# Kernel optimization log

Measured on AMD Instinct MI355X. Metric: run time of the kernel, lower is better.

Reference implementation:

```python
import jax, jax.numpy as jnp
import numpy as np

B, T, N, M, L = 64, 256, 1024, 1024, 2


def setup_inputs() -> dict:
    key = jax.random.key(0)
    ks = jax.random.split(key, 5)
    scale = 1.0 / np.sqrt(M)
    x = jax.random.normal(ks[0], (B, T, N), dtype=jnp.float32)
    h = jnp.zeros((L, B, M), dtype=jnp.float32)
    c = jnp.zeros((L, B, M), dtype=jnp.float32)
    Wx = jax.random.normal(ks[1], (L, 4 * M, N), dtype=jnp.float32) * scale
    Wh = jax.random.normal(ks[2], (L, 4 * M, M), dtype=jnp.float32) * scale
    b = jnp.zeros((L, 4 * M), dtype=jnp.float32)
    return {"x": x, "h": h, "c": c, "Wx": Wx, "Wh": Wh, "b": b}


def _lstm_stack(x, h0, c0, Wx, Wh, b):
    # x: [B,T,N]; h0,c0: [L,B,M]; Wx: [L,4M,N_or_M]; Wh: [L,4M,M]; b: [L,4M]
    num_layers = Wx.shape[0]

    def step(carry, xt):
        h, c = carry  # each [L,B,M]
        inp = xt      # [B,N]
        hs, cs = [], []
        for l in range(num_layers):
            gates = inp @ Wx[l].T + h[l] @ Wh[l].T + b[l]  # [B,4M]
            i, f, g, o = jnp.split(gates, 4, axis=-1)
            i = jax.nn.sigmoid(i)
            f = jax.nn.sigmoid(f)
            g = jnp.tanh(g)
            o = jax.nn.sigmoid(o)
            cl = f * c[l] + i * g
            hl = o * jnp.tanh(cl)
            hs.append(hl)
            cs.append(cl)
            inp = hl
        h_new = jnp.stack(hs)
        c_new = jnp.stack(cs)
        return (h_new, c_new), h_new[-1]

    xt = jnp.swapaxes(x, 0, 1)  # [T,B,N]
    (h_last, c_last), outs = jax.lax.scan(step, (h0, c0), xt)
    outs = jnp.swapaxes(outs, 0, 1)  # [B,T,M]
    return outs, h_last, c_last


def reference(x, h, c, Wx, Wh, b):
    return _lstm_stack(x, h, c, Wx, Wh, b)
```

## Files before the change

### kernel.cpp

```cpp
#include <hip/hip_runtime.h>


#define T_STEPS 256
#define B_SZ 64
#define M_SZ 1024
#define N_SZ 1024
#define G4M 4096
#define BM 65536
#define RING 32
#define OUTS ((size_t)16777216)

typedef short short8 __attribute__((ext_vector_type(8)));
typedef float f32x4 __attribute__((ext_vector_type(4)));

static __device__ __forceinline__ unsigned short f2bf(float f) {
  union { float f; unsigned int u; } v; v.f = f;
  unsigned int u = v.u;
  unsigned int r = (u + 0x7FFFu + ((u >> 16) & 1u)) >> 16;
  return (unsigned short)r;
}

static __device__ __forceinline__ float sigf(float x) {
  return 1.f / (1.f + __expf(-x));
}
static __device__ __forceinline__ float tanhfast(float x) {
  return 2.f / (1.f + __expf(-2.f * x)) - 1.f;
}

static __device__ __forceinline__ short8 ld16(const unsigned short* p) {
  return *reinterpret_cast<const short8*>(p);
}

static __device__ __forceinline__ void store_wt16(void* p, f32x4 v) {
  asm volatile("global_store_dwordx4 %0, %1, off sc0 sc1" :: "v"(p), "v"(v) : "memory");
}

static __device__ __forceinline__ int xcc_id() {
  int v;
  asm volatile("s_getreg_b32 %0, hwreg(HW_REG_XCC_ID)" : "=s"(v));
  return v & 7;
}

__global__ void convert_x_kernel(const float* __restrict__ x,
                                 unsigned short* __restrict__ xb, int n4) {
  int i = blockIdx.x * blockDim.x + threadIdx.x;
  int stride = gridDim.x * blockDim.x;
  for (; i < n4; i += stride) {
    float4 v = reinterpret_cast<const float4*>(x)[i];
    ushort4 o;
    o.x = f2bf(v.x); o.y = f2bf(v.y); o.z = f2bf(v.z); o.w = f2bf(v.w);
    reinterpret_cast<ushort4*>(xb)[i] = o;
  }
}

__global__ void init_h_kernel(const float* __restrict__ h,
                              unsigned short* __restrict__ h0r,
                              unsigned short* __restrict__ h1r) {
  int i = blockIdx.x * blockDim.x + threadIdx.x;
  h0r[(size_t)(RING - 1) * BM + i] = f2bf(h[i]);
  h1r[(size_t)(RING - 1) * BM + i] = f2bf(h[BM + i]);
}

__global__ __launch_bounds__(1024, 4) void lstm_persistent(
    const unsigned short* __restrict__ xb,
    const float* __restrict__ c_in,
    const float* __restrict__ Wx,
    const float* __restrict__ Wh,
    const float* __restrict__ bias,
    float* __restrict__ out,
    unsigned short* __restrict__ h0r,
    unsigned short* __restrict__ h1r,
    int* bar) {
  __shared__ short8 sW[2][2][32][64];
  __shared__ f32x4 red1[12][64];
  __shared__ f32x4 red2[12][64];

  const int cu = blockIdx.x;
  const int tid = threadIdx.x;
  const int lane = tid & 63;
  const int w = tid >> 6;
  const int g = cu & 1;
  const int cuL = cu >> 1;
  const int src = w >> 3;
  const int kh = (w >> 2) & 1;
  const int bt = w & 3;
  const int q = lane >> 4;
  const int bl = lane & 15;
  const int bg = bt * 16 + bl;
  const int mbase = cuL * 8;
  const int xcd = xcc_id();
  const bool owner = (w < 4);

  unsigned short* hr_own = g ? h1r : h0r;

  {
    const float* baseX = Wx + (size_t)g * G4M * N_SZ;
    const float* baseH = Wh + (size_t)g * G4M * M_SZ;
#pragma unroll
    for (int mat = 0; mat < 2; ++mat) {
      const float* base = mat ? baseH : baseX;
#pragma unroll
      for (int mg = 0; mg < 2; ++mg) {
        for (int s = tid; s < 32 * 64; s += 1024) {
          int kt = s >> 6, ls = s & 63;
          int r = ls & 15;
          int k0 = kt * 32 + (ls >> 4) * 8;
          int j = (r >> 2) * 1024 + mbase + mg * 4 + (r & 3);
          const float* srcp = base + (size_t)j * 1024 + k0;
          float4 a = reinterpret_cast<const float4*>(srcp)[0];
          float4 b2 = reinterpret_cast<const float4*>(srcp)[1];
          short8 wv;
          wv[0] = (short)f2bf(a.x); wv[1] = (short)f2bf(a.y);
          wv[2] = (short)f2bf(a.z); wv[3] = (short)f2bf(a.w);
          wv[4] = (short)f2bf(b2.x); wv[5] = (short)f2bf(b2.y);
          wv[6] = (short)f2bf(b2.z); wv[7] = (short)f2bf(b2.w);
          sW[mat][mg][kt][ls] = wv;
        }
      }
    }
  }

  bool leader = false;
  if (tid == 0) {
    int expected = 0;
    leader = __hip_atomic_compare_exchange_strong(
        bar + 16 * (66 + g * 8 + xcd), &expected, cu + 1, __ATOMIC_RELAXED,
        __ATOMIC_RELAXED, __HIP_MEMORY_SCOPE_AGENT);
  }
  __syncthreads();

  float c_st[2][4] = {{0.f,0.f,0.f,0.f},{0.f,0.f,0.f,0.f}};
  float bs[2][4] = {{0.f,0.f,0.f,0.f},{0.f,0.f,0.f,0.f}};
  if (owner) {
#pragma unroll
    for (int mg = 0; mg < 2; ++mg)
#pragma unroll
      for (int e = 0; e < 4; ++e) {
        c_st[mg][e] = c_in[g * BM + bg * M_SZ + mbase + mg * 4 + e];
        bs[mg][e] = bias[g * G4M + q * 1024 + mbase + mg * 4 + e];
      }
  }

  const int ko = q * 8;
  const int ktb = kh * 16;
  int* prog0 = bar + 16 * 82;
  int* prog1 = bar + 16 * 83;

  if (g == 1 && tid == 0) {
    int guard = 0;
    while (__hip_atomic_load(prog0, __ATOMIC_RELAXED, __HIP_MEMORY_SCOPE_AGENT) < 1) {
      __builtin_amdgcn_s_sleep(1);
      if (++guard > (1 << 22)) break;
    }
  }
  __syncthreads();

  for (int k = 0; k < T_STEPS; ++k) {
    const int rs = (k + RING - 1) & (RING - 1);
    const int wslot = k & (RING - 1);

    const unsigned short* ip;
    if (src == 0) {
      ip = g ? (h0r + (size_t)wslot * BM + (size_t)bg * M_SZ)
             : (xb + ((size_t)bg * T_STEPS + k) * N_SZ);
    } else {
      ip = hr_own + (size_t)rs * BM + (size_t)bg * M_SZ;
    }

    f32x4 acc0 = { 0.f, 0.f, 0.f, 0.f };
    f32x4 acc1 = { 0.f, 0.f, 0.f, 0.f };
    if (owner) {
#pragma unroll
      for (int e = 0; e < 4; ++e) { acc0[e] = bs[0][e]; acc1[e] = bs[1][e]; }
    }

    short8 f[16];
#pragma unroll
    for (int j = 0; j < 16; ++j) f[j] = ld16(ip + (ktb + j) * 32 + ko);
    asm volatile("" ::
      "v"(f[0]), "v"(f[1]), "v"(f[2]), "v"(f[3]),
      "v"(f[4]), "v"(f[5]), "v"(f[6]), "v"(f[7]),
      "v"(f[8]), "v"(f[9]), "v"(f[10]), "v"(f[11]),
      "v"(f[12]), "v"(f[13]), "v"(f[14]), "v"(f[15]));
    __builtin_amdgcn_sched_barrier(0);
#pragma unroll
    for (int j = 0; j < 16; ++j) {
      int kt = ktb + j;
      acc0 = __builtin_amdgcn_mfma_f32_16x16x32_bf16(sW[src][0][kt][lane], f[j], acc0, 0, 0, 0);
      acc1 = __builtin_amdgcn_mfma_f32_16x16x32_bf16(sW[src][1][kt][lane], f[j], acc1, 0, 0, 0);
    }

    if (!owner) {
      int idx = (w >> 2) - 1;
      red1[idx * 4 + bt][lane] = acc0;
      red2[idx * 4 + bt][lane] = acc1;
    }
    asm volatile("s_waitcnt lgkmcnt(0)" ::: "memory");
    __builtin_amdgcn_s_barrier();
    __builtin_amdgcn_sched_barrier(0);

    if (owner) {
      f32x4 tot[2];
      tot[0] = acc0 + red1[bt][lane] + red1[4 + bt][lane] + red1[8 + bt][lane];
      tot[1] = acc1 + red2[bt][lane] + red2[4 + bt][lane] + red2[8 + bt][lane];
      float hv[2][4];
#pragma unroll
      for (int mg = 0; mg < 2; ++mg) {
#pragma unroll
        for (int e = 0; e < 4; ++e) {
          float ge_i = __shfl(tot[mg][e], bl);
          float ge_f = __shfl(tot[mg][e], bl + 16);
          float ge_g = __shfl(tot[mg][e], bl + 32);
          float ge_o = __shfl(tot[mg][e], bl + 48);
          float gi = sigf(ge_i), gf = sigf(ge_f);
          float gg = tanhfast(ge_g), go = sigf(ge_o);
          float c = gf * c_st[mg][e] + gi * gg;
          c_st[mg][e] = c;
          hv[mg][e] = go * tanhfast(c);
        }
      }
      if (q == 0) {
#pragma unroll
        for (int mg = 0; mg < 2; ++mg) {
          unsigned short* hdst = hr_own + (size_t)wslot * BM +
                                 (size_t)bg * M_SZ + mbase + mg * 4;
          unsigned long long hb =
              (unsigned long long)f2bf(hv[mg][0]) |
              ((unsigned long long)f2bf(hv[mg][1]) << 16) |
              ((unsigned long long)f2bf(hv[mg][2]) << 32) |
              ((unsigned long long)f2bf(hv[mg][3]) << 48);
          __hip_atomic_store((unsigned long long*)hdst, hb, __ATOMIC_RELAXED,
                             __HIP_MEMORY_SCOPE_AGENT);
          if (g == 1) {
            f32x4 ov = { hv[mg][0], hv[mg][1], hv[mg][2], hv[mg][3] };
            store_wt16(out + ((size_t)bg * T_STEPS + k) * M_SZ + mbase + mg * 4, ov);
          }
          if (k == T_STEPS - 1) {
            f32x4 hf = { hv[mg][0], hv[mg][1], hv[mg][2], hv[mg][3] };
            f32x4 cf = { c_st[mg][0], c_st[mg][1], c_st[mg][2], c_st[mg][3] };
            store_wt16(out + OUTS + (size_t)g * BM + (size_t)bg * M_SZ + mbase + mg * 4, hf);
            store_wt16(out + OUTS + 2 * (size_t)BM + (size_t)g * BM +
                       (size_t)bg * M_SZ + mbase + mg * 4, cf);
          }
        }
      }
    }

    {
      const int target = k + 1;
      const bool invstep = ((k & (RING - 1)) == (RING - 1));
      if (owner)
        asm volatile("s_waitcnt vmcnt(0)" ::: "memory");
      __builtin_amdgcn_s_barrier();
      if (tid == 0) {
        int* leaf = bar + 16 * (g * 16 + (cuL & 15));
        int* root = bar + 16 * (32 + g);
        int prev = __hip_atomic_fetch_add(leaf, 1, __ATOMIC_RELAXED, __HIP_MEMORY_SCOPE_AGENT);
        if ((prev & 7) == 7) {
          int pr2 = __hip_atomic_fetch_add(root, 1, __ATOMIC_RELAXED, __HIP_MEMORY_SCOPE_AGENT);
          if ((pr2 & 15) == 15) {
            __hip_atomic_store(bar + 16 * (82 + g), target, __ATOMIC_RELAXED,
                               __HIP_MEMORY_SCOPE_AGENT);
#pragma unroll
            for (int xx = 0; xx < 8; ++xx)
              __hip_atomic_store(bar + 16 * (34 + g * 8 + xx), target,
                                 __ATOMIC_RELAXED, __HIP_MEMORY_SCOPE_AGENT);
          }
        }
        int guard = 0;
        int* rel  = bar + 16 * (34 + g * 8 + xcd);
        int* relB = bar + 16 * (50 + g * 8 + xcd);
        while (__hip_atomic_load(rel, __ATOMIC_RELAXED, __HIP_MEMORY_SCOPE_AGENT) < target) {
          __builtin_amdgcn_s_sleep(1);
          if (++guard > (1 << 22)) break;
        }
        if (g == 1 && k + 1 < T_STEPS) {
          int need = (k + 2 < T_STEPS + 1) ? (k + 2) : T_STEPS;
          guard = 0;
          while (__hip_atomic_load(prog0, __ATOMIC_RELAXED, __HIP_MEMORY_SCOPE_AGENT) < need) {
            __builtin_amdgcn_s_sleep(1);
            if (++guard > (1 << 22)) break;
          }
        } else if (g == 0 && k + 1 >= RING && k + 1 < T_STEPS) {
          int need = k - 30;
          guard = 0;
          while (__hip_atomic_load(prog1, __ATOMIC_RELAXED, __HIP_MEMORY_SCOPE_AGENT) < need) {
            __builtin_amdgcn_s_sleep(1);
            if (++guard > (1 << 22)) break;
          }
        }
        if (invstep) {
          if (leader) {
            asm volatile("buffer_inv sc0 sc1\n\ts_waitcnt vmcnt(0)" ::: "memory");
            __hip_atomic_store(relB, target, __ATOMIC_RELAXED, __HIP_MEMORY_SCOPE_AGENT);
          } else {
            guard = 0;
            while (__hip_atomic_load(relB, __ATOMIC_RELAXED, __HIP_MEMORY_SCOPE_AGENT) < target) {
              __builtin_amdgcn_s_sleep(1);
              if (++guard > (1 << 22)) break;
            }
            asm volatile("buffer_inv sc0\n\ts_waitcnt vmcnt(0)" ::: "memory");
          }
        }
      }
      __builtin_amdgcn_s_barrier();
      __builtin_amdgcn_sched_barrier(0);
    }
  }
}

extern "C" void kernel_launch(void* const* d_in, const int* in_sizes, int n_in,
                              void* d_out, int out_size, void* d_ws, size_t ws_size,
                              hipStream_t stream) {
  (void)in_sizes; (void)n_in; (void)out_size; (void)ws_size;
  const float* x  = (const float*)d_in[0];
  const float* h  = (const float*)d_in[1];
  const float* c  = (const float*)d_in[2];
  const float* Wx = (const float*)d_in[3];
  const float* Wh = (const float*)d_in[4];
  const float* b  = (const float*)d_in[5];
  float* out = (float*)d_out;

  char* ws = (char*)d_ws;
  int* bar = (int*)ws;
  unsigned short* h0r = (unsigned short*)(ws + 8192);
  unsigned short* h1r = (unsigned short*)(ws + 8192 + (size_t)RING * BM * 2);
  unsigned short* xb  = (unsigned short*)(ws + 8192 + (size_t)RING * BM * 4);

  (void)hipMemsetAsync(ws, 0, 8192, stream);
  convert_x_kernel<<<2048, 256, 0, stream>>>(x, xb, (B_SZ * T_STEPS * N_SZ) / 4);
  init_h_kernel<<<256, 256, 0, stream>>>(h, h0r, h1r);
  lstm_persistent<<<256, 1024, 0, stream>>>(xb, c, Wx, Wh, b, out, h0r, h1r, bar);
}
```

Measured before the change: 3.151 ms.

## Split LSTM into four pipelined domains with separate input-projection producers

```diff
diff --git a/kernel.cpp b/kernel.cpp
--- a/kernel.cpp
+++ b/kernel.cpp
@@ -8,6 +8,7 @@
 #define G4M 4096
 #define BM 65536
 #define RING 32
+#define GSTRIDE ((size_t)262144)
 #define OUTS ((size_t)16777216)
 
 typedef short short8 __attribute__((ext_vector_type(8)));
@@ -19,22 +20,22 @@
   unsigned int r = (u + 0x7FFFu + ((u >> 16) & 1u)) >> 16;
   return (unsigned short)r;
 }
-
+static __device__ __forceinline__ float bf2f(unsigned int us) {
+  union { unsigned int u; float f; } v; v.u = (us & 0xFFFFu) << 16;
+  return v.f;
+}
 static __device__ __forceinline__ float sigf(float x) {
   return 1.f / (1.f + __expf(-x));
 }
 static __device__ __forceinline__ float tanhfast(float x) {
   return 2.f / (1.f + __expf(-2.f * x)) - 1.f;
 }
-
 static __device__ __forceinline__ short8 ld16(const unsigned short* p) {
   return *reinterpret_cast<const short8*>(p);
 }
-
 static __device__ __forceinline__ void store_wt16(void* p, f32x4 v) {
   asm volatile("global_store_dwordx4 %0, %1, off sc0 sc1" :: "v"(p), "v"(v) : "memory");
 }
-
 static __device__ __forceinline__ int xcc_id() {
   int v;
   asm volatile("s_getreg_b32 %0, hwreg(HW_REG_XCC_ID)" : "=s"(v));
@@ -61,7 +62,7 @@
   h1r[(size_t)(RING - 1) * BM + i] = f2bf(h[BM + i]);
 }
 
-__global__ __launch_bounds__(1024, 4) void lstm_persistent(
+__global__ __launch_bounds__(1024, 4) void lstm_pipeline(
     const unsigned short* __restrict__ xb,
     const float* __restrict__ c_in,
     const float* __restrict__ Wx,
@@ -70,52 +71,43 @@
     float* __restrict__ out,
     unsigned short* __restrict__ h0r,
     unsigned short* __restrict__ h1r,
+    unsigned short* __restrict__ g0x,
+    unsigned short* __restrict__ g1x,
     int* bar) {
-  __shared__ short8 sW[2][2][32][64];
-  __shared__ f32x4 red1[12][64];
-  __shared__ f32x4 red2[12][64];
+  __shared__ short8 sW[4][32][64];
 
   const int cu = blockIdx.x;
   const int tid = threadIdx.x;
   const int lane = tid & 63;
   const int w = tid >> 6;
-  const int g = cu & 1;
-  const int cuL = cu >> 1;
-  const int src = w >> 3;
-  const int kh = (w >> 2) & 1;
-  const int bt = w & 3;
+  const int dom = cu & 3;
+  const int cuD = cu >> 2;
+  const int lay = dom & 1;
+  const bool serial = (dom < 2);
   const int q = lane >> 4;
   const int bl = lane & 15;
-  const int bg = bt * 16 + bl;
-  const int mbase = cuL * 8;
+  const int ko = q * 8;
   const int xcd = xcc_id();
-  const bool owner = (w < 4);
-
-  unsigned short* hr_own = g ? h1r : h0r;
 
   {
-    const float* baseX = Wx + (size_t)g * G4M * N_SZ;
-    const float* baseH = Wh + (size_t)g * G4M * M_SZ;
-#pragma unroll
-    for (int mat = 0; mat < 2; ++mat) {
-      const float* base = mat ? baseH : baseX;
-#pragma unroll
-      for (int mg = 0; mg < 2; ++mg) {
-        for (int s = tid; s < 32 * 64; s += 1024) {
-          int kt = s >> 6, ls = s & 63;
-          int r = ls & 15;
-          int k0 = kt * 32 + (ls >> 4) * 8;
-          int j = (r >> 2) * 1024 + mbase + mg * 4 + (r & 3);
-          const float* srcp = base + (size_t)j * 1024 + k0;
-          float4 a = reinterpret_cast<const float4*>(srcp)[0];
-          float4 b2 = reinterpret_cast<const float4*>(srcp)[1];
-          short8 wv;
-          wv[0] = (short)f2bf(a.x); wv[1] = (short)f2bf(a.y);
-          wv[2] = (short)f2bf(a.z); wv[3] = (short)f2bf(a.w);
-          wv[4] = (short)f2bf(b2.x); wv[5] = (short)f2bf(b2.y);
-          wv[6] = (short)f2bf(b2.z); wv[7] = (short)f2bf(b2.w);
-          sW[mat][mg][kt][ls] = wv;
-        }
+    const float* base = serial ? (Wh + (size_t)lay * G4M * M_SZ)
+                               : (Wx + (size_t)lay * G4M * N_SZ);
+#pragma unroll
+    for (int idx4 = 0; idx4 < 4; ++idx4) {
+      for (int s = tid; s < 32 * 64; s += 1024) {
+        int kt = s >> 6, ls = s & 63, r = ls & 15;
+        int k0 = kt * 32 + (ls >> 4) * 8;
+        int j = serial ? (idx4 * 1024 + cuD * 16 + r)
+                       : (cuD * 64 + idx4 * 16 + r);
+        const float* sp = base + (size_t)j * 1024 + k0;
+        float4 a = reinterpret_cast<const float4*>(sp)[0];
+        float4 b2 = reinterpret_cast<const float4*>(sp)[1];
+        short8 wv;
+        wv[0] = (short)f2bf(a.x); wv[1] = (short)f2bf(a.y);
+        wv[2] = (short)f2bf(a.z); wv[3] = (short)f2bf(a.w);
+        wv[4] = (short)f2bf(b2.x); wv[5] = (short)f2bf(b2.y);
+        wv[6] = (short)f2bf(b2.z); wv[7] = (short)f2bf(b2.w);
+        sW[idx4][kt][ls] = wv;
       }
     }
   }
@@ -124,172 +116,241 @@
   if (tid == 0) {
     int expected = 0;
     leader = __hip_atomic_compare_exchange_strong(
-        bar + 16 * (66 + g * 8 + xcd), &expected, cu + 1, __ATOMIC_RELAXED,
+        bar + 16 * (100 + dom * 8 + xcd), &expected, cu + 1, __ATOMIC_RELAXED,
         __ATOMIC_RELAXED, __HIP_MEMORY_SCOPE_AGENT);
   }
   __syncthreads();
 
-  float c_st[2][4] = {{0.f,0.f,0.f,0.f},{0.f,0.f,0.f,0.f}};
-  float bs[2][4] = {{0.f,0.f,0.f,0.f},{0.f,0.f,0.f,0.f}};
-  if (owner) {
-#pragma unroll
-    for (int mg = 0; mg < 2; ++mg)
-#pragma unroll
-      for (int e = 0; e < 4; ++e) {
-        c_st[mg][e] = c_in[g * BM + bg * M_SZ + mbase + mg * 4 + e];
-        bs[mg][e] = bias[g * G4M + q * 1024 + mbase + mg * 4 + e];
-      }
-  }
-
-  const int ko = q * 8;
-  const int ktb = kh * 16;
-  int* prog0 = bar + 16 * 82;
-  int* prog1 = bar + 16 * 83;
-
-  if (g == 1 && tid == 0) {
+  int* prog0  = bar + 16 * 132;
+  int* prog1  = bar + 16 * 133;
+  int* progB0 = bar + 16 * 134;
+  int* progB1 = bar + 16 * 135;
+
+  if (tid == 0) {
     int guard = 0;
-    while (__hip_atomic_load(prog0, __ATOMIC_RELAXED, __HIP_MEMORY_SCOPE_AGENT) < 1) {
-      __builtin_amdgcn_s_sleep(1);
-      if (++guard > (1 << 22)) break;
+    if (dom == 0) {
+      while (__hip_atomic_load(progB0, __ATOMIC_RELAXED, __HIP_MEMORY_SCOPE_AGENT) < 1) {
+        __builtin_amdgcn_s_sleep(1); if (++guard > (1 << 22)) break;
+      }
+    } else if (dom == 1) {
+      while (__hip_atomic_load(progB1, __ATOMIC_RELAXED, __HIP_MEMORY_SCOPE_AGENT) < 1) {
+        __builtin_amdgcn_s_sleep(1); if (++guard > (1 << 22)) break;
+      }
+    } else if (dom == 3) {
+      while (__hip_atomic_load(prog0, __ATOMIC_RELAXED, __HIP_MEMORY_SCOPE_AGENT) < 1) {
+        __builtin_amdgcn_s_sleep(1); if (++guard > (1 << 22)) break;
+      }
     }
   }
   __syncthreads();
 
-  for (int k = 0; k < T_STEPS; ++k) {
-    const int rs = (k + RING - 1) & (RING - 1);
-    const int wslot = k & (RING - 1);
-
-    const unsigned short* ip;
-    if (src == 0) {
-      ip = g ? (h0r + (size_t)wslot * BM + (size_t)bg * M_SZ)
-             : (xb + ((size_t)bg * T_STEPS + k) * N_SZ);
-    } else {
-      ip = hr_own + (size_t)rs * BM + (size_t)bg * M_SZ;
+  int* myleaf = bar + 16 * (dom * 8 + (cuD & 7));
+  int* myroot = bar + 16 * (32 + dom);
+  int* myprog = bar + 16 * (132 + dom);
+  int* rel  = bar + 16 * (36 + dom * 8 + xcd);
+  int* relB = bar + 16 * (68 + dom * 8 + xcd);
+
+  if (serial) {
+    unsigned short* hr = lay ? h1r : h0r;
+    unsigned short* gr = lay ? g1x : g0x;
+    const int bt = w & 3;
+    const int bg = bt * 16 + bl;
+    const int mloc = cuD * 16 + q * 4;
+    float c_st[4] = {0.f, 0.f, 0.f, 0.f};
+    if (w < 4) {
+#pragma unroll
+      for (int e = 0; e < 4; ++e)
+        c_st[e] = c_in[lay * BM + bg * M_SZ + mloc + e];
     }
 
-    f32x4 acc0 = { 0.f, 0.f, 0.f, 0.f };
-    f32x4 acc1 = { 0.f, 0.f, 0.f, 0.f };
-    if (owner) {
-#pragma unroll
-      for (int e = 0; e < 4; ++e) { acc0[e] = bs[0][e]; acc1[e] = bs[1][e]; }
-    }
-
-    short8 f[16];
-#pragma unroll
-    for (int j = 0; j < 16; ++j) f[j] = ld16(ip + (ktb + j) * 32 + ko);
-    asm volatile("" ::
-      "v"(f[0]), "v"(f[1]), "v"(f[2]), "v"(f[3]),
-      "v"(f[4]), "v"(f[5]), "v"(f[6]), "v"(f[7]),
-      "v"(f[8]), "v"(f[9]), "v"(f[10]), "v"(f[11]),
-      "v"(f[12]), "v"(f[13]), "v"(f[14]), "v"(f[15]));
-    __builtin_amdgcn_sched_barrier(0);
-#pragma unroll
-    for (int j = 0; j < 16; ++j) {
-      int kt = ktb + j;
-      acc0 = __builtin_amdgcn_mfma_f32_16x16x32_bf16(sW[src][0][kt][lane], f[j], acc0, 0, 0, 0);
-      acc1 = __builtin_amdgcn_mfma_f32_16x16x32_bf16(sW[src][1][kt][lane], f[j], acc1, 0, 0, 0);
-    }
-
-    if (!owner) {
-      int idx = (w >> 2) - 1;
-      red1[idx * 4 + bt][lane] = acc0;
-      red2[idx * 4 + bt][lane] = acc1;
-    }
-    asm volatile("s_waitcnt lgkmcnt(0)" ::: "memory");
-    __builtin_amdgcn_s_barrier();
-    __builtin_amdgcn_sched_barrier(0);
-
-    if (owner) {
-      f32x4 tot[2];
-      tot[0] = acc0 + red1[bt][lane] + red1[4 + bt][lane] + red1[8 + bt][lane];
-      tot[1] = acc1 + red2[bt][lane] + red2[4 + bt][lane] + red2[8 + bt][lane];
-      float hv[2][4];
-#pragma unroll
-      for (int mg = 0; mg < 2; ++mg) {
+    for (int k = 0; k < T_STEPS; ++k) {
+      const int rs = (k + RING - 1) & (RING - 1);
+      const int wsl = k & (RING - 1);
+      if (w < 4) {
+        const unsigned short* hp = hr + (size_t)rs * BM + (size_t)bg * M_SZ;
+        short8 f[32];
+#pragma unroll
+        for (int j = 0; j < 32; ++j) f[j] = ld16(hp + j * 32 + ko);
+        asm volatile("" ::
+          "v"(f[0]), "v"(f[1]), "v"(f[2]), "v"(f[3]), "v"(f[4]), "v"(f[5]),
+          "v"(f[6]), "v"(f[7]), "v"(f[8]), "v"(f[9]), "v"(f[10]), "v"(f[11]),
+          "v"(f[12]), "v"(f[13]), "v"(f[14]), "v"(f[15]));
+        asm volatile("" ::
+          "v"(f[16]), "v"(f[17]), "v"(f[18]), "v"(f[19]), "v"(f[20]), "v"(f[21]),
+          "v"(f[22]), "v"(f[23]), "v"(f[24]), "v"(f[25]), "v"(f[26]), "v"(f[27]),
+          "v"(f[28]), "v"(f[29]), "v"(f[30]), "v"(f[31]));
+        const unsigned short* gp = gr + (size_t)wsl * GSTRIDE + (size_t)bg * G4M + mloc;
+        unsigned long long gv0 = *(const unsigned long long*)(gp);
+        unsigned long long gv1 = *(const unsigned long long*)(gp + 1024);
+        unsigned long long gv2 = *(const unsigned long long*)(gp + 2048);
+        unsigned long long gv3 = *(const unsigned long long*)(gp + 3072);
+        __builtin_amdgcn_sched_barrier(0);
+        f32x4 a0 = {0.f,0.f,0.f,0.f}, a1 = {0.f,0.f,0.f,0.f};
+        f32x4 a2 = {0.f,0.f,0.f,0.f}, a3 = {0.f,0.f,0.f,0.f};
+#pragma unroll
+        for (int j = 0; j < 32; ++j) {
+          a0 = __builtin_amdgcn_mfma_f32_16x16x32_bf16(sW[0][j][lane], f[j], a0, 0, 0, 0);
+          a1 = __builtin_amdgcn_mfma_f32_16x16x32_bf16(sW[1][j][lane], f[j], a1, 0, 0, 0);
+          a2 = __builtin_amdgcn_mfma_f32_16x16x32_bf16(sW[2][j][lane], f[j], a2, 0, 0, 0);
+          a3 = __builtin_amdgcn_mfma_f32_16x16x32_bf16(sW[3][j][lane], f[j], a3, 0, 0, 0);
+        }
+        float hv[4];
 #pragma unroll
         for (int e = 0; e < 4; ++e) {
-          float ge_i = __shfl(tot[mg][e], bl);
-          float ge_f = __shfl(tot[mg][e], bl + 16);
-          float ge_g = __shfl(tot[mg][e], bl + 32);
-          float ge_o = __shfl(tot[mg][e], bl + 48);
-          float gi = sigf(ge_i), gf = sigf(ge_f);
-          float gg = tanhfast(ge_g), go = sigf(ge_o);
-          float c = gf * c_st[mg][e] + gi * gg;
-          c_st[mg][e] = c;
-          hv[mg][e] = go * tanhfast(c);
-        }
-      }
-      if (q == 0) {
-#pragma unroll
-        for (int mg = 0; mg < 2; ++mg) {
-          unsigned short* hdst = hr_own + (size_t)wslot * BM +
-                                 (size_t)bg * M_SZ + mbase + mg * 4;
-          unsigned long long hb =
-              (unsigned long long)f2bf(hv[mg][0]) |
-              ((unsigned long long)f2bf(hv[mg][1]) << 16) |
-              ((unsigned long long)f2bf(hv[mg][2]) << 32) |
-              ((unsigned long long)f2bf(hv[mg][3]) << 48);
-          __hip_atomic_store((unsigned long long*)hdst, hb, __ATOMIC_RELAXED,
-                             __HIP_MEMORY_SCOPE_AGENT);
-          if (g == 1) {
-            f32x4 ov = { hv[mg][0], hv[mg][1], hv[mg][2], hv[mg][3] };
-            store_wt16(out + ((size_t)bg * T_STEPS + k) * M_SZ + mbase + mg * 4, ov);
-          }
-          if (k == T_STEPS - 1) {
-            f32x4 hf = { hv[mg][0], hv[mg][1], hv[mg][2], hv[mg][3] };
-            f32x4 cf = { c_st[mg][0], c_st[mg][1], c_st[mg][2], c_st[mg][3] };
-            store_wt16(out + OUTS + (size_t)g * BM + (size_t)bg * M_SZ + mbase + mg * 4, hf);
-            store_wt16(out + OUTS + 2 * (size_t)BM + (size_t)g * BM +
-                       (size_t)bg * M_SZ + mbase + mg * 4, cf);
-          }
-        }
-      }
-    }
-
-    {
-      const int target = k + 1;
-      const bool invstep = ((k & (RING - 1)) == (RING - 1));
-      if (owner)
+          float ig = a0[e] + bf2f((unsigned int)(gv0 >> (16 * e)));
+          float fg = a1[e] + bf2f((unsigned int)(gv1 >> (16 * e)));
+          float gg = a2[e] + bf2f((unsigned int)(gv2 >> (16 * e)));
+          float og = a3[e] + bf2f((unsigned int)(gv3 >> (16 * e)));
+          float c = sigf(fg) * c_st[e] + sigf(ig) * tanhfast(gg);
+          c_st[e] = c;
+          hv[e] = sigf(og) * tanhfast(c);
+        }
+        unsigned long long hb =
+            (unsigned long long)f2bf(hv[0]) |
+            ((unsigned long long)f2bf(hv[1]) << 16) |
+            ((unsigned long long)f2bf(hv[2]) << 32) |
+            ((unsigned long long)f2bf(hv[3]) << 48);
+        __hip_atomic_store(
+            (unsigned long long*)(hr + (size_t)wsl * BM + (size_t)bg * M_SZ + mloc),
+            hb, __ATOMIC_RELAXED, __HIP_MEMORY_SCOPE_AGENT);
+        if (lay == 1) {
+          f32x4 ov = { hv[0], hv[1], hv[2], hv[3] };
+          store_wt16(out + ((size_t)bg * T_STEPS + k) * M_SZ + mloc, ov);
+        }
+        if (k == T_STEPS - 1) {
+          f32x4 hf = { hv[0], hv[1], hv[2], hv[3] };
+          f32x4 cf = { c_st[0], c_st[1], c_st[2], c_st[3] };
+          store_wt16(out + OUTS + (size_t)lay * BM + (size_t)bg * M_SZ + mloc, hf);
+          store_wt16(out + OUTS + 2 * (size_t)BM + (size_t)lay * BM +
+                     (size_t)bg * M_SZ + mloc, cf);
+        }
         asm volatile("s_waitcnt vmcnt(0)" ::: "memory");
+      }
       __builtin_amdgcn_s_barrier();
       if (tid == 0) {
-        int* leaf = bar + 16 * (g * 16 + (cuL & 15));
-        int* root = bar + 16 * (32 + g);
-        int prev = __hip_atomic_fetch_add(leaf, 1, __ATOMIC_RELAXED, __HIP_MEMORY_SCOPE_AGENT);
+        const int target = k + 1;
+        int prev = __hip_atomic_fetch_add(myleaf, 1, __ATOMIC_RELAXED, __HIP_MEMORY_SCOPE_AGENT);
         if ((prev & 7) == 7) {
-          int pr2 = __hip_atomic_fetch_add(root, 1, __ATOMIC_RELAXED, __HIP_MEMORY_SCOPE_AGENT);
-          if ((pr2 & 15) == 15) {
-            __hip_atomic_store(bar + 16 * (82 + g), target, __ATOMIC_RELAXED,
-                               __HIP_MEMORY_SCOPE_AGENT);
+          int pr2 = __hip_atomic_fetch_add(myroot, 1, __ATOMIC_RELAXED, __HIP_MEMORY_SCOPE_AGENT);
+          if ((pr2 & 7) == 7) {
+            __hip_atomic_store(myprog, target, __ATOMIC_RELAXED, __HIP_MEMORY_SCOPE_AGENT);
 #pragma unroll
             for (int xx = 0; xx < 8; ++xx)
-              __hip_atomic_store(bar + 16 * (34 + g * 8 + xx), target,
+              __hip_atomic_store(bar + 16 * (36 + dom * 8 + xx), target,
                                  __ATOMIC_RELAXED, __HIP_MEMORY_SCOPE_AGENT);
           }
         }
         int guard = 0;
-        int* rel  = bar + 16 * (34 + g * 8 + xcd);
-        int* relB = bar + 16 * (50 + g * 8 + xcd);
         while (__hip_atomic_load(rel, __ATOMIC_RELAXED, __HIP_MEMORY_SCOPE_AGENT) < target) {
           __builtin_amdgcn_s_sleep(1);
           if (++guard > (1 << 22)) break;
         }
-        if (g == 1 && k + 1 < T_STEPS) {
-          int need = (k + 2 < T_STEPS + 1) ? (k + 2) : T_STEPS;
+        if (k + 1 < T_STEPS) {
+          int* need_p = (dom == 0) ? progB0 : progB1;
           guard = 0;
-          while (__hip_atomic_load(prog0, __ATOMIC_RELAXED, __HIP_MEMORY_SCOPE_AGENT) < need) {
+          while (__hip_atomic_load(need_p, __ATOMIC_RELAXED, __HIP_MEMORY_SCOPE_AGENT) < k + 2) {
             __builtin_amdgcn_s_sleep(1);
             if (++guard > (1 << 22)) break;
           }
-        } else if (g == 0 && k + 1 >= RING && k + 1 < T_STEPS) {
-          int need = k - 30;
+          if (dom == 0 && k + 1 >= RING) {
+            guard = 0;
+            while (__hip_atomic_load(progB1, __ATOMIC_RELAXED, __HIP_MEMORY_SCOPE_AGENT) < k - 30) {
+              __builtin_amdgcn_s_sleep(1);
+              if (++guard > (1 << 22)) break;
+            }
+          }
+        }
+        if ((k & (RING - 1)) == (RING - 1)) {
+          if (leader) {
+            asm volatile("buffer_inv sc0 sc1\n\ts_waitcnt vmcnt(0)" ::: "memory");
+            __hip_atomic_store(relB, target, __ATOMIC_RELAXED, __HIP_MEMORY_SCOPE_AGENT);
+          } else {
+            guard = 0;
+            while (__hip_atomic_load(relB, __ATOMIC_RELAXED, __HIP_MEMORY_SCOPE_AGENT) < target) {
+              __builtin_amdgcn_s_sleep(1);
+              if (++guard > (1 << 22)) break;
+            }
+            asm volatile("buffer_inv sc0\n\ts_waitcnt vmcnt(0)" ::: "memory");
+          }
+        }
+      }
+      __builtin_amdgcn_s_barrier();
+      __builtin_amdgcn_sched_barrier(0);
+    }
+  } else {
+    unsigned short* gr = lay ? g1x : g0x;
+    const int rt = w >> 2, bt = w & 3;
+    const int bg = bt * 16 + bl;
+    const int rowb = cuD * 64 + rt * 16 + q * 4;
+    float bsv[4];
+#pragma unroll
+    for (int e = 0; e < 4; ++e) bsv[e] = bias[lay * G4M + rowb + e];
+
+    for (int k = 0; k < T_STEPS; ++k) {
+      const int wsl = k & (RING - 1);
+      const unsigned short* ip =
+          lay ? (h0r + (size_t)wsl * BM + (size_t)bg * M_SZ)
+              : (xb + ((size_t)bg * T_STEPS + k) * N_SZ);
+      short8 f[32];
+#pragma unroll
+      for (int j = 0; j < 32; ++j) f[j] = ld16(ip + j * 32 + ko);
+      asm volatile("" ::
+        "v"(f[0]), "v"(f[1]), "v"(f[2]), "v"(f[3]), "v"(f[4]), "v"(f[5]),
+        "v"(f[6]), "v"(f[7]), "v"(f[8]), "v"(f[9]), "v"(f[10]), "v"(f[11]),
+        "v"(f[12]), "v"(f[13]), "v"(f[14]), "v"(f[15]));
+      asm volatile("" ::
+        "v"(f[16]), "v"(f[17]), "v"(f[18]), "v"(f[19]), "v"(f[20]), "v"(f[21]),
+        "v"(f[22]), "v"(f[23]), "v"(f[24]), "v"(f[25]), "v"(f[26]), "v"(f[27]),
+        "v"(f[28]), "v"(f[29]), "v"(f[30]), "v"(f[31]));
+      __builtin_amdgcn_sched_barrier(0);
+      f32x4 acc = { bsv[0], bsv[1], bsv[2], bsv[3] };
+#pragma unroll
+      for (int j = 0; j < 32; ++j)
+        acc = __builtin_amdgcn_mfma_f32_16x16x32_bf16(sW[rt][j][lane], f[j], acc, 0, 0, 0);
+      unsigned long long gb =
+          (unsigned long long)f2bf(acc[0]) |
+          ((unsigned long long)f2bf(acc[1]) << 16) |
+          ((unsigned long long)f2bf(acc[2]) << 32) |
+          ((unsigned long long)f2bf(acc[3]) << 48);
+      __hip_atomic_store(
+          (unsigned long long*)(gr + (size_t)wsl * GSTRIDE + (size_t)bg * G4M + rowb),
+          gb, __ATOMIC_RELAXED, __HIP_MEMORY_SCOPE_AGENT);
+      asm volatile("s_waitcnt vmcnt(0)" ::: "memory");
+      __builtin_amdgcn_s_barrier();
+      if (tid == 0) {
+        const int target = k + 1;
+        int prev = __hip_atomic_fetch_add(myleaf, 1, __ATOMIC_RELAXED, __HIP_MEMORY_SCOPE_AGENT);
+        if ((prev & 7) == 7) {
+          int pr2 = __hip_atomic_fetch_add(myroot, 1, __ATOMIC_RELAXED, __HIP_MEMORY_SCOPE_AGENT);
+          if ((pr2 & 7) == 7) {
+            __hip_atomic_store(myprog, target, __ATOMIC_RELAXED, __HIP_MEMORY_SCOPE_AGENT);
+#pragma unroll
+            for (int xx = 0; xx < 8; ++xx)
+              __hip_atomic_store(bar + 16 * (36 + dom * 8 + xx), target,
+                                 __ATOMIC_RELAXED, __HIP_MEMORY_SCOPE_AGENT);
+          }
+        }
+        int guard = 0;
+        while (__hip_atomic_load(rel, __ATOMIC_RELAXED, __HIP_MEMORY_SCOPE_AGENT) < target) {
+          __builtin_amdgcn_s_sleep(1);
+          if (++guard > (1 << 22)) break;
+        }
+        if (dom == 3 && k + 1 < T_STEPS) {
           guard = 0;
-          while (__hip_atomic_load(prog1, __ATOMIC_RELAXED, __HIP_MEMORY_SCOPE_AGENT) < need) {
+          while (__hip_atomic_load(prog0, __ATOMIC_RELAXED, __HIP_MEMORY_SCOPE_AGENT) < k + 2) {
             __builtin_amdgcn_s_sleep(1);
             if (++guard > (1 << 22)) break;
           }
         }
-        if (invstep) {
+        if (k + 1 >= RING && k + 1 < T_STEPS) {
+          int* cons = (dom == 2) ? prog0 : prog1;
+          guard = 0;
+          while (__hip_atomic_load(cons, __ATOMIC_RELAXED, __HIP_MEMORY_SCOPE_AGENT) < k - 30) {
+            __builtin_amdgcn_s_sleep(1);
+            if (++guard > (1 << 22)) break;
+          }
+        }
+        if ((k & (RING - 1)) == (RING - 1)) {
           if (leader) {
             asm volatile("buffer_inv sc0 sc1\n\ts_waitcnt vmcnt(0)" ::: "memory");
             __hip_atomic_store(relB, target, __ATOMIC_RELAXED, __HIP_MEMORY_SCOPE_AGENT);
@@ -323,12 +384,17 @@
 
   char* ws = (char*)d_ws;
   int* bar = (int*)ws;
-  unsigned short* h0r = (unsigned short*)(ws + 8192);
-  unsigned short* h1r = (unsigned short*)(ws + 8192 + (size_t)RING * BM * 2);
-  unsigned short* xb  = (unsigned short*)(ws + 8192 + (size_t)RING * BM * 4);
-
-  (void)hipMemsetAsync(ws, 0, 8192, stream);
+  unsigned short* h0r = (unsigned short*)(ws + 16384);
+  unsigned short* h1r = (unsigned short*)(ws + 16384 + (size_t)RING * BM * 2);
+  unsigned short* g0x = (unsigned short*)(ws + 16384 + (size_t)RING * BM * 4);
+  unsigned short* g1x = (unsigned short*)(ws + 16384 + (size_t)RING * BM * 4 +
+                                          (size_t)RING * GSTRIDE * 2);
+  unsigned short* xb  = (unsigned short*)(ws + 16384 + (size_t)RING * BM * 4 +
+                                          (size_t)RING * GSTRIDE * 4);
+
+  (void)hipMemsetAsync(ws, 0, 16384, stream);
   convert_x_kernel<<<2048, 256, 0, stream>>>(x, xb, (B_SZ * T_STEPS * N_SZ) / 4);
   init_h_kernel<<<256, 256, 0, stream>>>(h, h0r, h1r);
-  lstm_persistent<<<256, 1024, 0, stream>>>(xb, c, Wx, Wh, b, out, h0r, h1r, bar);
-}
+  lstm_pipeline<<<256, 1024, 0, stream>>>(xb, c, Wx, Wh, b, out,
+                                          h0r, h1r, g0x, g1x, bar);
+}
```

New measurement: 11.63 ms. 3.69x slower.
